# Optimization experiments

Measured on AMD Instinct MI355X. Metric: run time of the kernel, lower is better.

Reference implementation:

```python
import jax, jax.numpy as jnp
import numpy as np

N_NODES = 50000
IN_FEATS = 256
OUT_DIM = 64
N_EDGES = 800000


def setup_inputs() -> dict:
    key = jax.random.key(0)
    k1, k2, k3, k4 = jax.random.split(key, 4)
    x = jax.random.normal(k1, (N_NODES, IN_FEATS), dtype=jnp.float32)
    edge_index = jax.random.randint(k2, (2, N_EDGES), 0, N_NODES, dtype=jnp.int64)
    # Glorot-style init for the GCN weight, zeros bias (as in PyG GCNConv)
    scale = jnp.sqrt(6.0 / (IN_FEATS + OUT_DIM)).astype(jnp.float32)
    W = jax.random.uniform(k3, (IN_FEATS, OUT_DIM), dtype=jnp.float32, minval=-1.0, maxval=1.0) * scale
    b = jnp.zeros((OUT_DIM,), dtype=jnp.float32)
    return {"x": x, "edge_index": edge_index, "W": W, "b": b}


def _gcn_relu(x, edge_index, W, b):
    n = x.shape[0]
    # linear transform first (PyG GCNConv): h = x @ W
    h = x @ W  # [N, out_dim]
    # add self-loops
    loops = jnp.arange(n, dtype=edge_index.dtype)
    src = jnp.concatenate([edge_index[0], loops])  # [E+N]
    dst = jnp.concatenate([edge_index[1], loops])
    # symmetric degree normalization: deg over target index with unit weights
    deg = jax.ops.segment_sum(jnp.ones_like(dst, dtype=h.dtype), dst, num_segments=n)
    deg_inv_sqrt = jnp.where(deg > 0, jax.lax.rsqrt(jnp.maximum(deg, 1e-12)), 0.0)
    norm = deg_inv_sqrt[src] * deg_inv_sqrt[dst]  # [E+N]
    # gather source features, scale, scatter-add at destination
    msg = h[src] * norm[:, None]  # [E+N, out_dim]
    agg = jax.ops.segment_sum(msg, dst, num_segments=n)  # [N, out_dim]
    return jax.nn.relu(agg + b)


def reference(x, edge_index, W, b):
    return _gcn_relu(x, edge_index, W, b)
```

## Files before the change

kernel.cpp:

```cpp
#include <hip/hip_runtime.h>
#include <hip/hip_fp16.h>

#define INF    256
#define OUTF   64
#define TSH    7
#define TNODE  128
#define NBMAX  512
#define CAP    3584
#define MS_T   512
#define MS_EPT 8

typedef __attribute__((ext_vector_type(8))) short bf16x8;
typedef __attribute__((ext_vector_type(4))) float f32x4;

__device__ __forceinline__ short f2bf(float f) {
    union { float f; unsigned int u; } v; v.f = f;
    unsigned int u = v.u;
    u += 0x7FFFu + ((u >> 16) & 1u);
    return (short)(u >> 16);
}

__global__ void init_gcur_kernel(int* __restrict__ gcur, int nbuck) {
    int i = blockIdx.x * blockDim.x + threadIdx.x;
    if (i < nbuck) gcur[i] = i * CAP;
}

__global__ __launch_bounds__(MS_T) void msplit_kernel(
    const int* __restrict__ src, const int* __restrict__ dst,
    int* __restrict__ gcur, int* __restrict__ ebuk, int e, int nbuck)
{
    __shared__ int h[NBMAX], lb[NBMAX];
    const int t = threadIdx.x;
    for (int i = t; i < nbuck; i += MS_T) h[i] = 0;
    __syncthreads();

    const int base = blockIdx.x * (MS_T * MS_EPT);
    const int i0 = base + t * MS_EPT;
    int sv[MS_EPT], dl[MS_EPT], off[MS_EPT], bk[MS_EPT];

    if (i0 + MS_EPT <= e) {
        int4 s0 = *reinterpret_cast<const int4*>(src + i0);
        int4 s1 = *reinterpret_cast<const int4*>(src + i0 + 4);
        int4 d0 = *reinterpret_cast<const int4*>(dst + i0);
        int4 d1 = *reinterpret_cast<const int4*>(dst + i0 + 4);
        sv[0]=s0.x; sv[1]=s0.y; sv[2]=s0.z; sv[3]=s0.w;
        sv[4]=s1.x; sv[5]=s1.y; sv[6]=s1.z; sv[7]=s1.w;
        int dd[MS_EPT] = {d0.x,d0.y,d0.z,d0.w,d1.x,d1.y,d1.z,d1.w};
        #pragma unroll
        for (int k = 0; k < MS_EPT; ++k) {
            bk[k] = dd[k] >> TSH; dl[k] = dd[k] & (TNODE - 1);
            off[k] = atomicAdd(&h[bk[k]], 1);
        }
    } else {
        #pragma unroll
        for (int k = 0; k < MS_EPT; ++k) {
            int i = i0 + k;
            if (i < e) {
                int dd = dst[i];
                sv[k] = src[i]; bk[k] = dd >> TSH; dl[k] = dd & (TNODE - 1);
                off[k] = atomicAdd(&h[bk[k]], 1);
            } else bk[k] = -1;
        }
    }
    __syncthreads();
    for (int i = t; i < nbuck; i += MS_T) lb[i] = h[i] ? atomicAdd(&gcur[i], h[i]) : 0;
    __syncthreads();
    #pragma unroll
    for (int k = 0; k < MS_EPT; ++k) {
        if (bk[k] >= 0) {
            int pos = lb[bk[k]] + off[k];
            if (pos < (bk[k] + 1) * CAP)
                ebuk[pos] = (sv[k] & 0xFFFF) | (dl[k] << 16);
        }
    }
}

__global__ __launch_bounds__(256) void place_kernel(
    const int* __restrict__ gcur, const int* __restrict__ ebuk,
    unsigned short* __restrict__ ecol, int* __restrict__ rowptr,
    unsigned short* __restrict__ pcnt, float* __restrict__ dinv, int n)
{
    __shared__ int h[TNODE];
    __shared__ int lcur[TNODE];
    __shared__ unsigned short outb[CAP];

    const int b = blockIdx.x;
    const int t = threadIdx.x;
    const int nb0 = b << TSH;
    const int nn  = min(TNODE, n - nb0);
    const int beg = b * CAP;
    const int m   = min(gcur[b] - beg, CAP);

    if (t < TNODE) h[t] = 0;
    __syncthreads();
    for (int i = t; i < m; i += 256)
        atomicAdd(&h[(ebuk[beg + i] >> 16) & (TNODE - 1)], 1);
    __syncthreads();

    int v = (t < TNODE) ? h[t] : 0;
    if (t < TNODE) lcur[t] = v;
    __syncthreads();
    #pragma unroll
    for (int o = 1; o < TNODE; o <<= 1) {
        int add = (t < TNODE && t >= o) ? lcur[t - o] : 0;
        __syncthreads();
        if (t < TNODE) lcur[t] += add;
        __syncthreads();
    }
    if (t < TNODE) {
        int excl = lcur[t] - v;
        if (t < nn) {
            rowptr[nb0 + t] = beg + excl;
            pcnt[nb0 + t]   = (unsigned short)v;
            dinv[nb0 + t]   = rsqrtf((float)(v + 1));
        }
        lcur[t] = excl;
    }
    __syncthreads();

    for (int i = t; i < m; i += 256) {
        int p = ebuk[beg + i];
        int o = atomicAdd(&lcur[(p >> 16) & (TNODE - 1)], 1);
        outb[o] = (unsigned short)(p & 0xFFFF);
    }
    __syncthreads();
    for (int i = t; i < m; i += 256) ecol[beg + i] = outb[i];
}

__global__ __launch_bounds__(256, 2) void gemm_mfma_kernel(
    const float* __restrict__ x, const float* __restrict__ W,
    const float* __restrict__ dinv, __half* __restrict__ hp16,
    int n, int ntiles, int wstride)
{
    __shared__ char smem[65536];
    const int lane = threadIdx.x & 63;
    const int wv   = threadIdx.x >> 6;
    const int wid  = blockIdx.x * 4 + wv;
    const int lg   = lane >> 4;
    const int lr   = lane & 15;
    char* buf0 = smem + wv * 16384;
    char* buf1 = buf0 + 8192;

    bf16x8 breg[4][8];
    #pragma unroll
    for (int ct = 0; ct < 4; ++ct) {
        #pragma unroll
        for (int ks = 0; ks < 8; ++ks) {
            const float* wp = W + (size_t)(ks * 32 + lg * 8) * OUTF + ct * 16 + lr;
            bf16x8 f;
            #pragma unroll
            for (int j = 0; j < 8; ++j)
                f[j] = f2bf(wp[(size_t)j * OUTF]);
            breg[ct][ks] = f;
        }
    }

    auto stage_half = [&](const float* xrow0, char* buf) {
        #pragma unroll
        for (int i = 0; i < 8; ++i) {
            int row  = i * 2 + (lane >> 5);
            int colb = (((lane & 31) << 4) ^ ((row & 7) << 4));
            const float* srcp = xrow0 + (size_t)row * INF + (colb >> 2);
            __builtin_amdgcn_global_load_lds(
                (const __attribute__((address_space(1))) void*)srcp,
                (__attribute__((address_space(3))) void*)(buf + i * 1024),
                16, 0, 0);
        }
        asm volatile("" ::: "memory");
    };

    auto compute_half = [&](const char* buf, int khbase,
                            f32x4& acc0, f32x4& acc1, f32x4& acc2, f32x4& acc3) {
        const int m = (lr & 7) << 4;
        #pragma unroll
        for (int ksl = 0; ksl < 4; ++ksl) {
            int logical = lr * 512 + ksl * 128 + lg * 32;
            float4 a0 = *reinterpret_cast<const float4*>(buf + (logical ^ m));
            float4 a1 = *reinterpret_cast<const float4*>(buf + ((logical + 16) ^ m));
            bf16x8 af;
            af[0] = f2bf(a0.x); af[1] = f2bf(a0.y); af[2] = f2bf(a0.z); af[3] = f2bf(a0.w);
            af[4] = f2bf(a1.x); af[5] = f2bf(a1.y); af[6] = f2bf(a1.z); af[7] = f2bf(a1.w);
            acc0 = __builtin_amdgcn_mfma_f32_16x16x32_bf16(af, breg[0][khbase + ksl], acc0, 0, 0, 0);
            acc1 = __builtin_amdgcn_mfma_f32_16x16x32_bf16(af, breg[1][khbase + ksl], acc1, 0, 0, 0);
            acc2 = __builtin_amdgcn_mfma_f32_16x16x32_bf16(af, breg[2][khbase + ksl], acc2, 0, 0, 0);
            acc3 = __builtin_amdgcn_mfma_f32_16x16x32_bf16(af, breg[3][khbase + ksl], acc3, 0, 0, 0);
        }
    };

    for (int t = wid; t < ntiles; t += wstride) {
        const float* xt = x + (size_t)t * 16 * INF;
        stage_half(xt, buf0);
        stage_half(xt + 128, buf1);

        f32x4 acc0 = {0,0,0,0}, acc1 = {0,0,0,0}, acc2 = {0,0,0,0}, acc3 = {0,0,0,0};

        asm volatile("s_waitcnt vmcnt(8)" ::: "memory");
        compute_half(buf0, 0, acc0, acc1, acc2, acc3);

        asm volatile("s_waitcnt vmcnt(0)" ::: "memory");
        compute_half(buf1, 4, acc0, acc1, acc2, acc3);

        #pragma unroll
        for (int reg = 0; reg < 4; ++reg) {
            int row = t * 16 + lg * 4 + reg;
            float di = dinv[row];
            __half* op = hp16 + (size_t)row * OUTF + lr;
            op[0]  = __float2half(acc0[reg] * di);
            op[16] = __float2half(acc1[reg] * di);
            op[32] = __float2half(acc2[reg] * di);
            op[48] = __float2half(acc3[reg] * di);
        }
    }
}

__global__ __launch_bounds__(256) void aggregate_kernel(
    const int* __restrict__ rowptr, const unsigned short* __restrict__ pcnt,
    const unsigned short* __restrict__ ecol, const __half2* __restrict__ hp2,
    const float* __restrict__ dinv, const float* __restrict__ b,
    float* __restrict__ out, int n)
{
    int widx = (int)((blockIdx.x * (size_t)blockDim.x + threadIdx.x) >> 6);
    int lane = threadIdx.x & 63;
    int half = lane >> 5;
    int l    = lane & 31;
    if (widx >= n) return;

    float2 acc = make_float2(0.f, 0.f);
    if (half == 0) {
        float2 v = __half22float2(hp2[(size_t)widx * 32 + l]);
        acc.x = v.x; acc.y = v.y;
    }

    int beg = rowptr[widx];
    int end = beg + pcnt[widx];

    int j = beg + half;
    for (; j + 14 < end; j += 16) {
        int s0 = ecol[j];      int s1 = ecol[j + 2];
        int s2 = ecol[j + 4];  int s3 = ecol[j + 6];
        int s4 = ecol[j + 8];  int s5 = ecol[j + 10];
        int s6 = ecol[j + 12]; int s7 = ecol[j + 14];
        float2 v0 = __half22float2(hp2[(size_t)s0 * 32 + l]);
        float2 v1 = __half22float2(hp2[(size_t)s1 * 32 + l]);
        float2 v2 = __half22float2(hp2[(size_t)s2 * 32 + l]);
        float2 v3 = __half22float2(hp2[(size_t)s3 * 32 + l]);
        float2 v4 = __half22float2(hp2[(size_t)s4 * 32 + l]);
        float2 v5 = __half22float2(hp2[(size_t)s5 * 32 + l]);
        float2 v6 = __half22float2(hp2[(size_t)s6 * 32 + l]);
        float2 v7 = __half22float2(hp2[(size_t)s7 * 32 + l]);
        acc.x += v0.x + v1.x + v2.x + v3.x + v4.x + v5.x + v6.x + v7.x;
        acc.y += v0.y + v1.y + v2.y + v3.y + v4.y + v5.y + v6.y + v7.y;
    }
    for (; j < end; j += 2) {
        float2 v = __half22float2(hp2[(size_t)ecol[j] * 32 + l]);
        acc.x += v.x; acc.y += v.y;
    }

    float hx = __shfl(acc.x, lane | 32, 64);
    float hy = __shfl(acc.y, lane | 32, 64);
    if (half == 0) {
        float di = dinv[widx];
        float2 bb = reinterpret_cast<const float2*>(b)[l];
        float ox = fmaxf((acc.x + hx) * di + bb.x, 0.f);
        float oy = fmaxf((acc.y + hy) * di + bb.y, 0.f);
        reinterpret_cast<float2*>(out)[(size_t)widx * 32 + l] = make_float2(ox, oy);
    }
}

extern "C" void kernel_launch(void* const* d_in, const int* in_sizes, int n_in,
                              void* d_out, int out_size, void* d_ws, size_t ws_size,
                              hipStream_t stream) {
    const float* x    = (const float*)d_in[0];
    const int*   edge = (const int*)d_in[1];
    const float* W    = (const float*)d_in[2];
    const float* b    = (const float*)d_in[3];
    float* out = (float*)d_out;

    const int n = in_sizes[0] / INF;
    const int e = in_sizes[1] / 2;
    const int* src = edge;
    const int* dst = edge + e;
    const int nbuck = (n + TNODE - 1) >> TSH;

    char* wsc = (char*)d_ws;
    size_t off = 0;
    auto alloc = [&](size_t bytes) { char* p = wsc + off; off += (bytes + 511) & ~511ull; return p; };
    int*            gcur   = (int*)   alloc((size_t)NBMAX * 4);
    int*            rowptr = (int*)   alloc((size_t)n * 4);
    unsigned short* pcnt   = (unsigned short*)alloc((size_t)n * 2);
    float*          dinv   = (float*) alloc((size_t)n * 4);
    int*            ebuk   = (int*)   alloc((size_t)nbuck * CAP * 4);
    unsigned short* ecol   = (unsigned short*)alloc((size_t)nbuck * CAP * 2);
    __half*         hp16   = (__half*)alloc((size_t)n * OUTF * 2);

    init_gcur_kernel<<<2, 256, 0, stream>>>(gcur, nbuck);

    {
        int blocks = (e + MS_T * MS_EPT - 1) / (MS_T * MS_EPT);
        msplit_kernel<<<blocks, MS_T, 0, stream>>>(src, dst, gcur, ebuk, e, nbuck);
    }

    place_kernel<<<nbuck, 256, 0, stream>>>(gcur, ebuk, ecol, rowptr, pcnt, dinv, n);

    {
        const int ntiles = (n + 15) / 16;
        const int blocks = 512;
        gemm_mfma_kernel<<<blocks, 256, 0, stream>>>(x, W, dinv, hp16, n, ntiles, blocks * 4);
    }

    aggregate_kernel<<<(n + 3) / 4, 256, 0, stream>>>(rowptr, pcnt, ecol,
        reinterpret_cast<const __half2*>(hp16), dinv, b, out, n);
}
```

Before: 76.17 us.

## Split aggregation into two feature-plane passes with four edge groups per wave

The aggregation kernel now handles 32 of the 64 output features per launch and runs twice. Each wave splits into four 16-lane groups that walk interleaved edges and combine their partial sums with xor shuffles. With each pass touching only a 64-byte half of every source row, the gathered working set is halved, which should improve L2/MALL hit rates on the random gathers. The cost is an extra launch and re-reading rowptr, pcnt and ecol twice, and each gather now fetches only 64 bytes per row.

```diff
diff --git a/kernel.cpp b/kernel.cpp
--- a/kernel.cpp
+++ b/kernel.cpp
@@ -217,53 +217,51 @@
     const int* __restrict__ rowptr, const unsigned short* __restrict__ pcnt,
     const unsigned short* __restrict__ ecol, const __half2* __restrict__ hp2,
     const float* __restrict__ dinv, const float* __restrict__ b,
-    float* __restrict__ out, int n)
+    float* __restrict__ out, int n, int plane)
 {
     int widx = (int)((blockIdx.x * (size_t)blockDim.x + threadIdx.x) >> 6);
     int lane = threadIdx.x & 63;
-    int half = lane >> 5;
-    int l    = lane & 31;
+    int q = lane >> 4;
+    int l = lane & 15;
     if (widx >= n) return;
+    const int pl16 = plane << 4;
 
     float2 acc = make_float2(0.f, 0.f);
-    if (half == 0) {
-        float2 v = __half22float2(hp2[(size_t)widx * 32 + l]);
+    if (q == 0) {
+        float2 v = __half22float2(hp2[(size_t)widx * 32 + pl16 + l]);
         acc.x = v.x; acc.y = v.y;
     }
 
     int beg = rowptr[widx];
     int end = beg + pcnt[widx];
 
-    int j = beg + half;
-    for (; j + 14 < end; j += 16) {
-        int s0 = ecol[j];      int s1 = ecol[j + 2];
-        int s2 = ecol[j + 4];  int s3 = ecol[j + 6];
-        int s4 = ecol[j + 8];  int s5 = ecol[j + 10];
-        int s6 = ecol[j + 12]; int s7 = ecol[j + 14];
-        float2 v0 = __half22float2(hp2[(size_t)s0 * 32 + l]);
-        float2 v1 = __half22float2(hp2[(size_t)s1 * 32 + l]);
-        float2 v2 = __half22float2(hp2[(size_t)s2 * 32 + l]);
-        float2 v3 = __half22float2(hp2[(size_t)s3 * 32 + l]);
-        float2 v4 = __half22float2(hp2[(size_t)s4 * 32 + l]);
-        float2 v5 = __half22float2(hp2[(size_t)s5 * 32 + l]);
-        float2 v6 = __half22float2(hp2[(size_t)s6 * 32 + l]);
-        float2 v7 = __half22float2(hp2[(size_t)s7 * 32 + l]);
-        acc.x += v0.x + v1.x + v2.x + v3.x + v4.x + v5.x + v6.x + v7.x;
-        acc.y += v0.y + v1.y + v2.y + v3.y + v4.y + v5.y + v6.y + v7.y;
-    }
-    for (; j < end; j += 2) {
-        float2 v = __half22float2(hp2[(size_t)ecol[j] * 32 + l]);
+    int j = beg + q;
+    for (; j + 12 < end; j += 16) {
+        int s0 = ecol[j];      int s1 = ecol[j + 4];
+        int s2 = ecol[j + 8];  int s3 = ecol[j + 12];
+        float2 v0 = __half22float2(hp2[(size_t)s0 * 32 + pl16 + l]);
+        float2 v1 = __half22float2(hp2[(size_t)s1 * 32 + pl16 + l]);
+        float2 v2 = __half22float2(hp2[(size_t)s2 * 32 + pl16 + l]);
+        float2 v3 = __half22float2(hp2[(size_t)s3 * 32 + pl16 + l]);
+        acc.x += v0.x + v1.x + v2.x + v3.x;
+        acc.y += v0.y + v1.y + v2.y + v3.y;
+    }
+    for (; j < end; j += 4) {
+        float2 v = __half22float2(hp2[(size_t)ecol[j] * 32 + pl16 + l]);
         acc.x += v.x; acc.y += v.y;
     }
 
-    float hx = __shfl(acc.x, lane | 32, 64);
-    float hy = __shfl(acc.y, lane | 32, 64);
-    if (half == 0) {
+    acc.x += __shfl_xor(acc.x, 16, 64);
+    acc.y += __shfl_xor(acc.y, 16, 64);
+    acc.x += __shfl_xor(acc.x, 32, 64);
+    acc.y += __shfl_xor(acc.y, 32, 64);
+
+    if (q == 0) {
         float di = dinv[widx];
-        float2 bb = reinterpret_cast<const float2*>(b)[l];
-        float ox = fmaxf((acc.x + hx) * di + bb.x, 0.f);
-        float oy = fmaxf((acc.y + hy) * di + bb.y, 0.f);
-        reinterpret_cast<float2*>(out)[(size_t)widx * 32 + l] = make_float2(ox, oy);
+        float2 bb = reinterpret_cast<const float2*>(b)[pl16 + l];
+        float ox = fmaxf(acc.x * di + bb.x, 0.f);
+        float oy = fmaxf(acc.y * di + bb.y, 0.f);
+        reinterpret_cast<float2*>(out)[(size_t)widx * 32 + pl16 + l] = make_float2(ox, oy);
     }
 }
 
@@ -308,6 +306,11 @@
         gemm_mfma_kernel<<<blocks, 256, 0, stream>>>(x, W, dinv, hp16, n, ntiles, blocks * 4);
     }
 
-    aggregate_kernel<<<(n + 3) / 4, 256, 0, stream>>>(rowptr, pcnt, ecol,
-        reinterpret_cast<const __half2*>(hp16), dinv, b, out, n);
-}
+    {
+        int blocks = (n + 3) / 4;
+        aggregate_kernel<<<blocks, 256, 0, stream>>>(rowptr, pcnt, ecol,
+            reinterpret_cast<const __half2*>(hp16), dinv, b, out, n, 0);
+        aggregate_kernel<<<blocks, 256, 0, stream>>>(rowptr, pcnt, ecol,
+            reinterpret_cast<const __half2*>(hp16), dinv, b, out, n, 1);
+    }
+}
```

After: 92.42 us. +21.3%, slower.
